# Performance work log

Measured on AMD Instinct MI355X. Metric: run time of the kernel, lower is better.

The kernel has to match this reference:

```python
import jax, jax.numpy as jnp
import numpy as np
import math

B, T, H, W, C = 2, 8, 32, 32, 512
DEPTH = 2
HEADS = 16
GH = 8            # global FAVOR+ heads (first GH heads, as in performer-pytorch)
DH = C // HEADS   # 32
WIN = C // 8      # 64 = local window size
FF = 2 * C
NB_F = int(DH * math.log(DH))  # 110 random features (performer default)


def _ortho_proj(m, d, rng):
    # gaussian orthogonal random matrix, scaling=0 (row norms ~ chi(d))
    blocks = []
    for _ in range(m // d + 1):
        q, _ = np.linalg.qr(rng.standard_normal((d, d)))
        blocks.append(q.T)
    Q = np.concatenate(blocks, 0)[:m]
    mult = np.linalg.norm(rng.standard_normal((m, d)), axis=1)
    return (mult[:, None] * Q).astype(np.float32)


def setup_inputs():
    rng = np.random.default_rng(0)
    g = lambda *s: jnp.asarray(rng.standard_normal(s) * 0.02, jnp.float32)
    z = lambda *s: jnp.zeros(s, jnp.float32)
    o = lambda *s: jnp.ones(s, jnp.float32)
    p = {}
    p["x"] = jnp.asarray(rng.standard_normal((B, T, H, W, C)), jnp.float32)
    p["ln1_g"], p["ln1_b"] = o(DEPTH, C), z(DEPTH, C)
    p["Wq"], p["bq"] = g(DEPTH, C, C), z(DEPTH, C)
    p["Wk"], p["bk"] = g(DEPTH, C, C), z(DEPTH, C)
    p["Wv"], p["bv"] = g(DEPTH, C, C), z(DEPTH, C)
    p["Wo"], p["bo"] = g(DEPTH, C, C), z(DEPTH, C)
    p["proj"] = jnp.asarray(np.stack([_ortho_proj(NB_F, DH, rng) for _ in range(DEPTH)]))
    p["ln2_g"], p["ln2_b"] = o(DEPTH, C), z(DEPTH, C)
    p["W1"], p["b1"] = g(DEPTH, C, FF), z(DEPTH, FF)
    p["W2"], p["b2"] = g(DEPTH, FF, C), z(DEPTH, C)
    return p


def _ln(x, g, b):
    m = x.mean(-1, keepdims=True)
    v = x.var(-1, keepdims=True)
    return (x - m) / jnp.sqrt(v + 1e-5) * g + b


def _softmax_kernel(x, proj, is_query):
    # FAVOR+ positive softmax features. x: [b,h,n,d], proj: [m,d]
    d = x.shape[-1]
    m = proj.shape[0]
    dn = d ** -0.25
    dd = jnp.einsum('bhnd,md->bhnm', x * dn, proj)
    diag = jnp.sum(x * x, -1, keepdims=True) * 0.5 * (dn * dn)
    if is_query:
        stab = jnp.max(dd, axis=-1, keepdims=True)
    else:
        stab = jnp.max(dd, axis=(-1, -2), keepdims=True)
    return (m ** -0.5) * (jnp.exp(dd - diag - stab) + 1e-4)


def _rot_half(x):
    x1, x2 = jnp.split(x, 2, axis=-1)
    return jnp.concatenate([-x2, x1], axis=-1)


def _local_attn(q, k, v, win=WIN):
    # non-causal sliding window, look_backward=1, look_forward=1
    b, hh, n, d = q.shape
    nw = n // win
    qb = q.reshape(b, hh, nw, win, d)
    kb = k.reshape(b, hh, nw, win, d)
    vb = v.reshape(b, hh, nw, win, d)

    def look(t):
        p = jnp.pad(t, ((0, 0), (0, 0), (1, 1), (0, 0), (0, 0)))
        return jnp.concatenate([p[:, :, :-2], p[:, :, 1:-1], p[:, :, 2:]], 3)

    kk, vv = look(kb), look(vb)
    posb = jnp.arange(n).reshape(nw, win)
    pp = jnp.pad(posb, ((1, 1), (0, 0)), constant_values=-1)
    kpos = jnp.concatenate([pp[:-2], pp[1:-1], pp[2:]], 1)
    mask = (kpos == -1)[None, None, :, None, :]
    s = jnp.einsum('bhwid,bhwjd->bhwij', qb * (d ** -0.5), kk)
    s = jnp.where(mask, -1e9, s)
    a = jax.nn.softmax(s, axis=-1)
    o = jnp.einsum('bhwij,bhwjd->bhwid', a, vv)
    return o.reshape(b, hh, n, d)


def _forward(x, ln1_g, ln1_b, Wq, bq, Wk, bk, Wv, bv, Wo, bo, proj, ln2_g, ln2_b, W1, b1, W2, b2):
    Bx, Tx, Hx, Wx, Cx = x.shape
    n = Tx * Hx * Wx
    h = x.reshape(Bx, n, Cx)
    # rotary rel-pos for local heads (local-attention rel_pos_emb_config)
    inv_freq = 1.0 / (10000.0 ** (jnp.arange(0, DH, 2, dtype=jnp.float32) / DH))
    freqs = jnp.arange(n, dtype=jnp.float32)[:, None] * inv_freq[None, :]
    emb = jnp.concatenate([freqs, freqs], -1)
    sin, cos = jnp.sin(emb), jnp.cos(emb)

    for l in range(DEPTH):
        y = _ln(h, ln1_g[l], ln1_b[l])
        q = (y @ Wq[l] + bq[l]).reshape(Bx, n, HEADS, DH).transpose(0, 2, 1, 3)
        k = (y @ Wk[l] + bk[l]).reshape(Bx, n, HEADS, DH).transpose(0, 2, 1, 3)
        v = (y @ Wv[l] + bv[l]).reshape(Bx, n, HEADS, DH).transpose(0, 2, 1, 3)
        gq, lq = q[:, :GH], q[:, GH:]
        gk, lk = k[:, :GH], k[:, GH:]
        gv, lv = v[:, :GH], v[:, GH:]
        # global: FAVOR+ linear attention
        qp = _softmax_kernel(gq, proj[l], True)
        kp = _softmax_kernel(gk, proj[l], False)
        Dinv = 1.0 / jnp.einsum('bhnm,bhm->bhn', qp, kp.sum(-2))
        ctx = jnp.einsum('bhnm,bhnd->bhmd', kp, gv)
        og = jnp.einsum('bhmd,bhnm,bhn->bhnd', ctx, qp, Dinv)
        # local: windowed attention with rotary pos emb
        lqr = lq * cos + _rot_half(lq) * sin
        lkr = lk * cos + _rot_half(lk) * sin
        ol = _local_attn(lqr, lkr, lv)
        o = jnp.concatenate([og, ol], 1).transpose(0, 2, 1, 3).reshape(Bx, n, Cx)
        h = h + o @ Wo[l] + bo[l]
        y = _ln(h, ln2_g[l], ln2_b[l])
        h = h + jax.nn.gelu(y @ W1[l] + b1[l], approximate=False) @ W2[l] + b2[l]
    return h.reshape(Bx, Tx, Hx, Wx, Cx)


def reference(x, ln1_g, ln1_b, Wq, bq, Wk, bk, Wv, bv, Wo, bo, proj, ln2_g, ln2_b, W1, b1, W2, b2):
    return _forward(x, ln1_g, ln1_b, Wq, bq, Wk, bk, Wv, bv, Wo, bo, proj, ln2_g, ln2_b, W1, b1, W2, b2)
```

## Files before the change

### kernel.cpp

```cpp
#include <hip/hip_runtime.h>
#include <math.h>

namespace {

constexpr int BATCH = 2;
constexpr int NTOK  = 8192;
constexpr int MROWS = 16384;
constexpr int C     = 512;
constexpr int GH    = 8;
constexpr int DH    = 32;
constexpr int WIN   = 64;
constexpr int NW    = 128;
constexpr int FF    = 1024;
constexpr int NBF   = 110;
constexpr int NBFP  = 128;

constexpr float F_DN     = 0.42044820762685725f;
constexpr float F_RNORM  = 0.09534625892455924f;
constexpr float F_LSCALE = 0.17677669529663687f;

typedef __attribute__((ext_vector_type(8))) short bf16x8;
typedef __attribute__((ext_vector_type(4))) float f32x4;

__device__ __forceinline__ ushort f2b(float f){
  unsigned u = __float_as_uint(f);
  unsigned r = u + 0x7FFFu + ((u >> 16) & 1u);
  return (ushort)(r >> 16);
}
__device__ __forceinline__ float b2f(ushort u){
  return __uint_as_float((unsigned)u << 16);
}

__device__ __forceinline__ void gload16(const void* g, void* l){
  __builtin_amdgcn_global_load_lds((const __attribute__((address_space(1))) void*)g,
                                   (__attribute__((address_space(3))) void*)l, 16, 0, 0);
}

__global__ void k_tables(float* __restrict__ cost, float* __restrict__ sint){
  int idx = blockIdx.x*256 + threadIdx.x;
  if (idx >= NTOK*16) return;
  int pos = idx >> 4, f = idx & 15;
  float inv = powf(10000.f, -(float)f/16.f);
  float ang = (float)pos * inv;
  cost[idx] = cosf(ang);
  sint[idx] = sinf(ang);
}

__global__ __launch_bounds__(256) void k_wcvt_all(const float* __restrict__ Wq, const float* __restrict__ Wk,
     const float* __restrict__ Wv, const float* __restrict__ Wo, const float* __restrict__ W1,
     const float* __restrict__ W2, ushort* __restrict__ wt){
  __shared__ float t[32][33];
  int id = blockIdx.x;
  int l = id >> 11;
  int r = id & 2047;
  const float* src; ushort* dst; int K, N, bx, by;
  if (r < 1024){
    int mat = r >> 8, tt = r & 255;
    bx = tt & 15; by = tt >> 4; K = 512; N = 512;
    src = ((mat == 0) ? Wq : (mat == 1) ? Wk : (mat == 2) ? Wv : Wo) + (size_t)l*262144;
    dst = wt + (size_t)l*2097152 + (size_t)mat*262144;
  } else if (r < 1536){
    int tt = r - 1024;
    bx = tt & 31; by = tt >> 5; K = 512; N = 1024;
    src = W1 + (size_t)l*524288;
    dst = wt + (size_t)l*2097152 + 1048576;
  } else {
    int tt = r - 1536;
    bx = tt & 15; by = tt >> 4; K = 1024; N = 512;
    src = W2 + (size_t)l*524288;
    dst = wt + (size_t)l*2097152 + 1572864;
  }
  int tx = threadIdx.x & 31, ty = threadIdx.x >> 5;
  #pragma unroll
  for (int rr = ty; rr < 32; rr += 8) t[rr][tx] = src[(size_t)(by*32+rr)*N + bx*32 + tx];
  __syncthreads();
  #pragma unroll
  for (int rr = ty; rr < 32; rr += 8) dst[(size_t)(bx*32+rr)*K + by*32 + tx] = f2b(t[tx][rr]);
}

__global__ __launch_bounds__(256) void k_ln(const float* __restrict__ x, const float* __restrict__ g,
                     const float* __restrict__ b, ushort* __restrict__ y){
  int row = blockIdx.x, t = threadIdx.x;
  const float* xr = x + (size_t)row*C;
  float2 v = *(const float2*)(xr + 2*t);
  float s = v.x + v.y, ss = v.x*v.x + v.y*v.y;
  #pragma unroll
  for (int o = 32; o; o >>= 1){ s += __shfl_down(s, o); ss += __shfl_down(ss, o); }
  __shared__ float rs[4], rss[4];
  int wv = t >> 6, ln = t & 63;
  if (ln == 0){ rs[wv] = s; rss[wv] = ss; }
  __syncthreads();
  float S = rs[0]+rs[1]+rs[2]+rs[3], SS = rss[0]+rss[1]+rss[2]+rss[3];
  float mean = S * (1.f/C);
  float var  = SS * (1.f/C) - mean*mean;
  float rstd = rsqrtf(var + 1e-5f);
  float2 gg = *(const float2*)(g + 2*t);
  float2 bb = *(const float2*)(b + 2*t);
  ushort2 ov;
  ov.x = f2b((v.x - mean)*rstd*gg.x + bb.x);
  ov.y = f2b((v.y - mean)*rstd*gg.y + bb.y);
  *(ushort2*)(y + (size_t)row*C + 2*t) = ov;
}

template<int ACT, int OBF, int QKV>
__global__ __launch_bounds__(256) void k_mgemm(const ushort* __restrict__ A, const ushort* __restrict__ Bt,
      const float* __restrict__ bias, const float* __restrict__ bias2, const float* __restrict__ bias3,
      const float* __restrict__ res, float* __restrict__ outf, ushort* __restrict__ outb,
      const float* __restrict__ cosT, const float* __restrict__ sinT, int Nd, int Kd){
  __shared__ ushort As[128*32];
  __shared__ ushort Bs[128*32];
  int tid = threadIdx.x;
  int lane = tid & 63, wave = tid >> 6;
  int wr = wave >> 1, wc = wave & 1;
  int gx = gridDim.x;
  int nwg = gx * (int)gridDim.y;
  int bid = (int)(blockIdx.y*gx + blockIdx.x);
  int swz = (bid & 7)*(nwg >> 3) + (bid >> 3);
  int row0 = (swz / gx)*128, col0 = (swz % gx)*128;
  f32x4 acc[4][4] = {};
  for (int k0 = 0; k0 < Kd; k0 += 32){
    __syncthreads();
    #pragma unroll
    for (int c = 0; c < 2; c++){
      int off = (wave*2 + c)*1024 + lane*16;
      int r = off >> 6, ke = (off & 63) >> 1;
      gload16(A  + (size_t)(row0 + r)*Kd + k0 + ke, (char*)As + (wave*2 + c)*1024);
      gload16(Bt + (size_t)(col0 + r)*Kd + k0 + ke, (char*)Bs + (wave*2 + c)*1024);
    }
    __syncthreads();
    bf16x8 af[4], bfr[4];
    #pragma unroll
    for (int m = 0; m < 4; m++)
      af[m] = *(const bf16x8*)((const char*)As + (wr*64 + m*16 + (lane&15))*64 + (lane>>4)*16);
    #pragma unroll
    for (int n = 0; n < 4; n++)
      bfr[n] = *(const bf16x8*)((const char*)Bs + (wc*64 + n*16 + (lane&15))*64 + (lane>>4)*16);
    #pragma unroll
    for (int m = 0; m < 4; m++)
      #pragma unroll
      for (int n = 0; n < 4; n++)
        acc[m][n] = __builtin_amdgcn_mfma_f32_16x16x32_bf16(af[m], bfr[n], acc[m][n], 0, 0, 0);
  }
  if (QKV){
    #pragma unroll
    for (int m = 0; m < 4; m++){
      int rbase = row0 + wr*64 + m*16 + (lane>>4)*4;
      #pragma unroll
      for (int np = 0; np < 2; np++){
        int n0 = 2*np, n1 = n0 + 1;
        int ccol = col0 + wc*64 + n0*16 + (lane&15);
        int bid2 = ccol >> 9;
        int cl  = ccol & 511;
        const float* bp = (bid2 == 0) ? bias : (bid2 == 1) ? bias2 : bias3;
        float b0 = bp[cl], b1 = bp[cl+16];
        bool dorope = (bid2 < 2) && (cl >= 256);
        ushort* obase = outb + (size_t)bid2*MROWS*C;
        int d = lane & 15;
        #pragma unroll
        for (int r = 0; r < 4; r++){
          int grow = rbase + r;
          float a  = acc[m][n0][r] + b0;
          float bb = acc[m][n1][r] + b1;
          if (dorope){
            int pos = grow & (NTOK-1);
            float cv = cosT[pos*16 + d], sv = sinT[pos*16 + d];
            float na = a*cv - bb*sv;
            float nb = bb*cv + a*sv;
            a = na; bb = nb;
          }
          obase[(size_t)grow*C + cl]      = f2b(a);
          obase[(size_t)grow*C + cl + 16] = f2b(bb);
        }
      }
    }
    return;
  }
  #pragma unroll
  for (int m = 0; m < 4; m++){
    int rbase = row0 + wr*64 + m*16 + (lane>>4)*4;
    #pragma unroll
    for (int n = 0; n < 4; n++){
      int ccol = col0 + wc*64 + n*16 + (lane&15);
      float bv = bias[ccol];
      #pragma unroll
      for (int r = 0; r < 4; r++){
        int grow = rbase + r;
        float vv = acc[m][n][r] + bv;
        if (ACT == 1) vv = 0.5f*vv*(1.f + erff(vv*0.7071067811865476f));
        if (res) vv += res[(size_t)grow*Nd + ccol];
        if (OBF) outb[(size_t)grow*Nd + ccol] = f2b(vv);
        else     outf[(size_t)grow*Nd + ccol] = vv;
      }
    }
  }
}

__global__ __launch_bounds__(256) void k_kpre2(const ushort* __restrict__ k, const float* __restrict__ proj,
        float* __restrict__ diag, float* __restrict__ bmax){
  int bh = blockIdx.x >> 5, chunk = blockIdx.x & 31;
  int b = bh >> 3, h = bh & 7;
  __shared__ __align__(16) ushort pl[NBFP*40];
  __shared__ float red[4];
  int tid = threadIdx.x, lane = tid & 63, wave = tid >> 6;
  int c = lane & 15, g = lane >> 4;
  for (int idx = tid; idx < NBFP*32; idx += 256){
    int f = idx >> 5, d = idx & 31;
    pl[f*40 + d] = (f < NBF) ? f2b(proj[idx]*F_DN) : (ushort)0;
  }
  __syncthreads();
  const ushort* kbase = k + ((size_t)b*NTOK + chunk*256)*C + h*DH;
  f32x4 zz = {0.f, 0.f, 0.f, 0.f};
  float mx = -1e30f;
  #pragma unroll
  for (int s = 0; s < 4; s++){
    bf16x8 af = *(const bf16x8*)(kbase + (size_t)(s*64 + wave*16 + c)*C + g*8);
    const ushort* ap = (const ushort*)&af;
    float sq = 0.f;
    #pragma unroll
    for (int j = 0; j < 8; j++){ float vv = b2f(ap[j]); sq += vv*vv; }
    sq += __shfl_xor(sq, 16);
    sq += __shfl_xor(sq, 32);
    if (g == 0) diag[bh*NTOK + chunk*256 + s*64 + wave*16 + c] = 0.5f*F_DN*F_DN*sq;
    #pragma unroll
    for (int ft = 0; ft < 8; ft++){
      bf16x8 bf = *(const bf16x8*)(pl + (ft*16 + c)*40 + g*8);
      f32x4 dd = __builtin_amdgcn_mfma_f32_16x16x32_bf16(af, bf, zz, 0, 0, 0);
      if (ft*16 + c < NBF)
        mx = fmaxf(mx, fmaxf(fmaxf(dd[0], dd[1]), fmaxf(dd[2], dd[3])));
    }
  }
  #pragma unroll
  for (int o = 1; o < 64; o <<= 1) mx = fmaxf(mx, __shfl_xor(mx, o));
  if (lane == 0) red[wave] = mx;
  __syncthreads();
  if (tid == 0) bmax[bh*32 + chunk] = fmaxf(fmaxf(red[0],red[1]), fmaxf(red[2],red[3]));
}

__global__ void k_redmax(const float* __restrict__ bmax, float* __restrict__ stabf){
  int bh = blockIdx.x, t = threadIdx.x;
  float v = (t < 32) ? bmax[bh*32 + t] : -1e30f;
  #pragma unroll
  for (int o = 32; o; o >>= 1) v = fmaxf(v, __shfl_down(v, o));
  if (t == 0) stabf[bh] = v;
}

__global__ __launch_bounds__(256) void k_ctx3(const ushort* __restrict__ k, const ushort* __restrict__ v,
        const float* __restrict__ proj, const float* __restrict__ diag, const float* __restrict__ stabf,
        float* __restrict__ ctxp, float* __restrict__ ksump){
  int bh = blockIdx.x >> 5, chunk = blockIdx.x & 31;
  int b = bh >> 3, h = bh & 7;
  __shared__ __align__(16) ushort pl[NBFP*40];
  __shared__ __align__(16) ushort Ps[NBFP*72];
  __shared__ __align__(16) ushort Vt[48*72];
  __shared__ float dgl[256];
  int tid = threadIdx.x;
  int lane = tid & 63, wave = tid >> 6;
  int c = lane & 15, g = lane >> 4;
  int i0 = chunk*256;

  for (int idx = tid; idx < NBFP*32; idx += 256){
    int f = idx >> 5, d = idx & 31;
    pl[f*40 + d] = (f < NBF) ? f2b(proj[f*32 + d]*F_DN) : (ushort)0;
  }
  dgl[tid] = diag[bh*NTOK + i0 + tid];
  for (int idx = tid; idx < 15*72; idx += 256) Vt[33*72 + idx] = 0;
  float stab_v = stabf[bh];

  const ushort* kbase = k + ((size_t)b*NTOK + i0)*C + h*DH;
  const ushort* vbase = v + ((size_t)b*NTOK + i0)*C + h*DH;
  f32x4 zz = {0.f, 0.f, 0.f, 0.f};
  f32x4 acc[2][3] = {};

  for (int s = 0; s < 4; s++){
    __syncthreads();
    {
      int r = tid >> 2, part = tid & 3;
      uint4 vv = *(const uint4*)(vbase + (size_t)(s*64 + r)*C + part*8);
      const ushort* vp = (const ushort*)&vv;
      #pragma unroll
      for (int j = 0; j < 8; j++) Vt[(part*8+j)*72 + r] = vp[j];
      if (tid < 64) Vt[32*72 + tid] = 0x3F80;
    }
    bf16x8 af = *(const bf16x8*)(kbase + (size_t)(s*64 + wave*16 + c)*C + g*8);
    #pragma unroll
    for (int ft = 0; ft < 8; ft++){
      bf16x8 bf = *(const bf16x8*)(pl + (ft*16 + c)*40 + g*8);
      f32x4 dd = __builtin_amdgcn_mfma_f32_16x16x32_bf16(af, bf, zz, 0, 0, 0);
      int feat = ft*16 + c;
      bool fvalid = feat < NBF;
      ushort pb[4];
      #pragma unroll
      for (int r = 0; r < 4; r++){
        float kp = 0.f;
        if (fvalid){
          float dg_ = dgl[s*64 + wave*16 + g*4 + r];
          kp = F_RNORM*(__expf(dd[r] - dg_ - stab_v) + 1e-4f);
        }
        pb[r] = f2b(kp);
      }
      uint2 pd;
      pd.x = (unsigned)pb[0] | ((unsigned)pb[1] << 16);
      pd.y = (unsigned)pb[2] | ((unsigned)pb[3] << 16);
      *(uint2*)(Ps + (ft*16 + c)*72 + wave*16 + g*4) = pd;
    }
    __syncthreads();
    #pragma unroll
    for (int i = 0; i < 2; i++){
      int ft = wave*2 + i;
      #pragma unroll
      for (int kk = 0; kk < 2; kk++){
        bf16x8 ap = *(const bf16x8*)(Ps + (ft*16 + c)*72 + kk*32 + g*8);
        #pragma unroll
        for (int nt = 0; nt < 3; nt++){
          bf16x8 bv = *(const bf16x8*)(Vt + (nt*16 + c)*72 + kk*32 + g*8);
          acc[i][nt] = __builtin_amdgcn_mfma_f32_16x16x32_bf16(ap, bv, acc[i][nt], 0, 0, 0);
        }
      }
    }
  }
  size_t pbase = (size_t)(bh*32 + chunk)*NBF;
  #pragma unroll
  for (int i = 0; i < 2; i++){
    int ftb = (wave*2 + i)*16;
    #pragma unroll
    for (int r = 0; r < 4; r++){
      int feat = ftb + g*4 + r;
      if (feat < NBF){
        #pragma unroll
        for (int nt = 0; nt < 2; nt++)
          ctxp[(pbase + feat)*DH + nt*16 + c] = acc[i][nt][r];
        if (c == 0) ksump[pbase + feat] = acc[i][2][r];
      }
    }
  }
}

__global__ void k_ctxred(const float* __restrict__ ctxp, const float* __restrict__ ksump,
                         float* __restrict__ ctx, float* __restrict__ ksum){
  int bh = blockIdx.x / NBF, m = blockIdx.x % NBF;
  int t = threadIdx.x;
  if (t < DH){
    float s = 0.f;
    for (int c = 0; c < 32; c++) s += ctxp[((size_t)(bh*32 + c)*NBF + m)*DH + t];
    ctx[((size_t)bh*NBF + m)*DH + t] = s;
  } else if (t == DH){
    float s = 0.f;
    for (int c = 0; c < 32; c++) s += ksump[(size_t)(bh*32 + c)*NBF + m];
    ksum[bh*NBF + m] = s;
  }
}

__global__ __launch_bounds__(256) void k_qattn3(const ushort* __restrict__ q, const float* __restrict__ proj,
        const float* __restrict__ ctx, const float* __restrict__ ksum, ushort* __restrict__ o){
  int bh = blockIdx.x >> 7, chunk = blockIdx.x & 127;
  int b = bh >> 3, h = bh & 7;
  __shared__ __align__(16) ushort pl[NBFP*40];
  __shared__ __align__(16) ushort ql[64*40];
  __shared__ __align__(16) ushort ctl[32*136];
  __shared__ __align__(16) ushort Ps[64*136];
  __shared__ float ksl[NBFP];
  __shared__ float dgl[64];
  __shared__ float dvl[64];
  int tid = threadIdx.x;
  int lane = tid & 63, wave = tid >> 6;
  int c = lane & 15, g = lane >> 4;
  int i0 = chunk*64;

  for (int idx = tid; idx < NBFP*32; idx += 256){
    int f = idx >> 5, d = idx & 31;
    pl[f*40 + d] = (f < NBF) ? f2b(proj[f*32 + d]*F_DN) : (ushort)0;
  }
  {
    int row = tid >> 2, part = tid & 3;
    uint4 qq = *(const uint4*)(q + (size_t)(b*NTOK + i0 + row)*C + h*DH + part*8);
    *(uint4*)(ql + row*40 + part*8) = qq;
    const ushort* qp_ = (const ushort*)&qq;
    float sq = 0.f;
    #pragma unroll
    for (int j = 0; j < 8; j++){ float vv = b2f(qp_[j]); sq += vv*vv; }
    sq += __shfl_xor(sq, 1);
    sq += __shfl_xor(sq, 2);
    if (part == 0) dgl[row] = 0.5f*F_DN*F_DN*sq;
  }
  for (int idx = tid; idx < 32*NBFP; idx += 256){
    int d = idx >> 7, f = idx & 127;
    float vv = (f < NBF) ? ctx[((size_t)bh*NBF + f)*DH + d] : 0.f;
    ctl[d*136 + f] = f2b(vv);
  }
  if (tid < NBFP) ksl[tid] = (tid < NBF) ? ksum[bh*NBF + tid] : 0.f;
  __syncthreads();

  f32x4 zz = {0.f, 0.f, 0.f, 0.f};
  bf16x8 qf = *(const bf16x8*)(ql + (wave*16 + c)*40 + g*8);
  f32x4 st[8];
  #pragma unroll
  for (int mt = 0; mt < 8; mt++){
    bf16x8 af = *(const bf16x8*)(pl + (mt*16 + c)*40 + g*8);
    st[mt] = __builtin_amdgcn_mfma_f32_16x16x32_bf16(af, qf, zz, 0, 0, 0);
  }
  float mx = -1e30f;
  #pragma unroll
  for (int mt = 0; mt < 8; mt++)
    #pragma unroll
    for (int r = 0; r < 4; r++){
      int feat = mt*16 + g*4 + r;
      if (feat < NBF) mx = fmaxf(mx, st[mt][r]);
    }
  mx = fmaxf(mx, __shfl_xor(mx, 16));
  mx = fmaxf(mx, __shfl_xor(mx, 32));
  float diagv = dgl[wave*16 + c];
  float dv = 0.f;
  #pragma unroll
  for (int mt = 0; mt < 8; mt++){
    ushort pb[4];
    #pragma unroll
    for (int r = 0; r < 4; r++){
      int feat = mt*16 + g*4 + r;
      float qp = 0.f;
      if (feat < NBF) qp = F_RNORM*(__expf(st[mt][r] - diagv - mx) + 1e-4f);
      ushort qb = f2b(qp);
      pb[r] = qb;
      dv += b2f(qb)*ksl[feat];
    }
    uint2 pd;
    pd.x = (unsigned)pb[0] | ((unsigned)pb[1] << 16);
    pd.y = (unsigned)pb[2] | ((unsigned)pb[3] << 16);
    *(uint2*)(Ps + (wave*16 + c)*136 + mt*16 + g*4) = pd;
  }
  dv += __shfl_xor(dv, 16);
  dv += __shfl_xor(dv, 32);
  if (g == 0) dvl[wave*16 + c] = 1.f/dv;
  __syncthreads();

  #pragma unroll
  for (int n = 0; n < 2; n++){
    f32x4 acc = zz;
    #pragma unroll
    for (int kk = 0; kk < 4; kk++){
      bf16x8 ap = *(const bf16x8*)(Ps  + (wave*16 + c)*136 + kk*32 + g*8);
      bf16x8 bc = *(const bf16x8*)(ctl + (n*16 + c)*136    + kk*32 + g*8);
      acc = __builtin_amdgcn_mfma_f32_16x16x32_bf16(ap, bc, acc, 0, 0, 0);
    }
    #pragma unroll
    for (int r = 0; r < 4; r++){
      int qrow = wave*16 + g*4 + r;
      float val = acc[r]*dvl[qrow];
      o[(size_t)(b*NTOK + i0 + qrow)*C + h*DH + n*16 + c] = f2b(val);
    }
  }
}

__global__ __launch_bounds__(256) void k_local2(const ushort* __restrict__ q, const ushort* __restrict__ k,
        const ushort* __restrict__ v, ushort* __restrict__ o){
  int blk = blockIdx.x;
  int w = blk & (NW-1);
  int rem = blk >> 7;
  int hl = rem & 7, b = rem >> 3;
  int hd = GH + hl;
  __shared__ __align__(16) ushort Ks[192*32];
  __shared__ __align__(16) ushort Vt[32*200];
  __shared__ __align__(16) ushort Ps[4*16*200];
  int tid = threadIdx.x;
  int lane = tid & 63, wave = tid >> 6;
  int c = lane & 15, g = lane >> 4;

  const ushort* kbase = k + (size_t)b*NTOK*C + hd*DH;
  const ushort* vbase = v + (size_t)b*NTOK*C + hd*DH;
  #pragma unroll
  for (int s = 0; s < 3; s++){
    int ch = tid + s*256;
    int row = ch >> 2, part = ch & 3;
    int kp = min(max((w-1)*WIN + row, 0), NTOK-1);
    gload16(kbase + (size_t)kp*C + part*8, (char*)Ks + (s*256 + wave*64)*16);
  }
  #pragma unroll
  for (int s = 0; s < 3; s++){
    int ch = tid + s*256;
    int row = ch >> 2, part = ch & 3;
    int kp = min(max((w-1)*WIN + row, 0), NTOK-1);
    uint4 vv = *(const uint4*)(vbase + (size_t)kp*C + part*8);
    const ushort* vp = (const ushort*)&vv;
    #pragma unroll
    for (int j = 0; j < 8; j++) Vt[(part*8+j)*200 + row] = vp[j];
  }
  int qrow = w*WIN + wave*16 + c;
  bf16x8 qf = *(const bf16x8*)(q + ((size_t)b*NTOK + qrow)*C + hd*DH + g*8);
  asm volatile("s_waitcnt vmcnt(0)" ::: "memory");
  __syncthreads();

  f32x4 zz = {0.f, 0.f, 0.f, 0.f};
  f32x4 st[12];
  #pragma unroll
  for (int t = 0; t < 12; t++){
    bf16x8 af = *(const bf16x8*)(Ks + (16*t + c)*32 + g*8);
    st[t] = __builtin_amdgcn_mfma_f32_16x16x32_bf16(af, qf, zz, 0, 0, 0);
  }
  int t0 = (w == 0) ? 4 : 0;
  int t1 = (w == NW-1) ? 8 : 12;
  float lsum = 0.f;
  ushort* pw = Ps + wave*3200 + c*200;
  #pragma unroll
  for (int t = 0; t < 12; t++){
    bool valid = (t >= t0) && (t < t1);
    float p0 = valid ? __expf(st[t][0]*F_LSCALE) : 0.f;
    float p1 = valid ? __expf(st[t][1]*F_LSCALE) : 0.f;
    float p2 = valid ? __expf(st[t][2]*F_LSCALE) : 0.f;
    float p3 = valid ? __expf(st[t][3]*F_LSCALE) : 0.f;
    lsum += (p0+p1)+(p2+p3);
    uint2 pd;
    pd.x = (unsigned)f2b(p0) | ((unsigned)f2b(p1) << 16);
    pd.y = (unsigned)f2b(p2) | ((unsigned)f2b(p3) << 16);
    *(uint2*)(pw + 16*t + 4*g) = pd;
  }
  lsum += __shfl_xor(lsum, 16);
  lsum += __shfl_xor(lsum, 32);

  f32x4 oc0 = zz, oc1 = zz;
  #pragma unroll
  for (int kb = 0; kb < 6; kb++){
    bf16x8 pf = *(const bf16x8*)(pw + kb*32 + g*8);
    bf16x8 v0 = *(const bf16x8*)(Vt + c*200 + kb*32 + g*8);
    bf16x8 v1 = *(const bf16x8*)(Vt + (16 + c)*200 + kb*32 + g*8);
    oc0 = __builtin_amdgcn_mfma_f32_16x16x32_bf16(v0, pf, oc0, 0, 0, 0);
    oc1 = __builtin_amdgcn_mfma_f32_16x16x32_bf16(v1, pf, oc1, 0, 0, 0);
  }
  float inv = 1.f/lsum;
  ushort* orow = o + ((size_t)b*NTOK + qrow)*C + hd*DH;
  uint2 w0, w1;
  w0.x = (unsigned)f2b(oc0[0]*inv) | ((unsigned)f2b(oc0[1]*inv) << 16);
  w0.y = (unsigned)f2b(oc0[2]*inv) | ((unsigned)f2b(oc0[3]*inv) << 16);
  w1.x = (unsigned)f2b(oc1[0]*inv) | ((unsigned)f2b(oc1[1]*inv) << 16);
  w1.y = (unsigned)f2b(oc1[2]*inv) | ((unsigned)f2b(oc1[3]*inv) << 16);
  *(uint2*)(orow + 4*g)      = w0;
  *(uint2*)(orow + 16 + 4*g) = w1;
}

}

extern "C" void kernel_launch(void* const* d_in, const int* in_sizes, int n_in,
                              void* d_out, int out_size, void* d_ws, size_t ws_size,
                              hipStream_t stream){
  (void)in_sizes; (void)n_in; (void)out_size; (void)ws_size;
  const float* x     = (const float*)d_in[0];
  const float* ln1_g = (const float*)d_in[1];
  const float* ln1_b = (const float*)d_in[2];
  const float* Wq    = (const float*)d_in[3];
  const float* bq    = (const float*)d_in[4];
  const float* Wk    = (const float*)d_in[5];
  const float* bk    = (const float*)d_in[6];
  const float* Wv    = (const float*)d_in[7];
  const float* bv    = (const float*)d_in[8];
  const float* Wo    = (const float*)d_in[9];
  const float* bo    = (const float*)d_in[10];
  const float* proj  = (const float*)d_in[11];
  const float* ln2_g = (const float*)d_in[12];
  const float* ln2_b = (const float*)d_in[13];
  const float* W1    = (const float*)d_in[14];
  const float* b1    = (const float*)d_in[15];
  const float* W2    = (const float*)d_in[16];
  const float* b2    = (const float*)d_in[17];

  float* h = (float*)d_out;
  const size_t MC = (size_t)MROWS*C;
  char* w = (char*)d_ws;
  auto alloc = [&](size_t bytes)->char*{ char* p = w; w += (bytes + 255) & ~(size_t)255; return p; };

  ushort* y16  = (ushort*)alloc(MC*2);
  ushort* qb16 = (ushort*)alloc(MC*2);
  ushort* kb16 = (ushort*)alloc(MC*2);
  ushort* vb16 = (ushort*)alloc(MC*2);
  ushort* o16  = (ushort*)alloc(MC*2);
  ushort* wt   = (ushort*)alloc((size_t)2*2097152*2);
  float*  cost = (float*) alloc((size_t)NTOK*16*4);
  float*  sint = (float*) alloc((size_t)NTOK*16*4);
  float*  diag = (float*) alloc((size_t)16*NTOK*4);
  float*  bmax = (float*) alloc(16*32*4);
  float*  stabf= (float*) alloc(16*4);
  float*  ctxb = (float*) alloc((size_t)16*NBF*DH*4);
  float*  ksum = (float*) alloc((size_t)16*NBF*4);

  ushort* mid16 = qb16;
  float*  ctxp  = (float*)o16;
  float*  ksump = ctxp + (size_t)16*32*NBF*DH;

  k_tables<<<(NTOK*16 + 255)/256, 256, 0, stream>>>(cost, sint);
  k_wcvt_all<<<4096, 256, 0, stream>>>(Wq, Wk, Wv, Wo, W1, W2, wt);

  dim3 blk(256);
  dim3 g512(4, 128);
  dim3 gqkv(12, 128);
  dim3 gff(8, 128);

  for (int l = 0; l < 2; l++){
    const float* pj = proj + (size_t)l*NBF*DH;
    ushort* wl  = wt + (size_t)l*2097152;
    ushort* wtq = wl;
    ushort* wto = wl +  786432;
    ushort* wt1 = wl + 1048576;
    ushort* wt2 = wl + 1572864;
    const float* hin = (l == 0) ? x : h;

    k_ln<<<MROWS, 256, 0, stream>>>(hin, ln1_g + l*C, ln1_b + l*C, y16);
    k_mgemm<0,1,1><<<gqkv, blk, 0, stream>>>(y16, wtq, bq + l*C, bk + l*C, bv + l*C,
                                             nullptr, nullptr, qb16, cost, sint, 1536, C);
    k_kpre2<<<16*32, 256, 0, stream>>>(kb16, pj, diag, bmax);
    k_redmax<<<16, 64, 0, stream>>>(bmax, stabf);
    k_ctx3<<<16*32, 256, 0, stream>>>(kb16, vb16, pj, diag, stabf, ctxp, ksump);
    k_ctxred<<<16*NBF, 64, 0, stream>>>(ctxp, ksump, ctxb, ksum);
    k_qattn3<<<16*128, 256, 0, stream>>>(qb16, pj, ctxb, ksum, o16);
    k_local2<<<BATCH*8*NW, 256, 0, stream>>>(qb16, kb16, vb16, o16);
    k_mgemm<0,0,0><<<g512, blk, 0, stream>>>(o16, wto, bo + l*C, nullptr, nullptr, hin, h, nullptr,
                                             nullptr, nullptr, C, C);
    k_ln<<<MROWS, 256, 0, stream>>>(h, ln2_g + l*C, ln2_b + l*C, y16);
    k_mgemm<1,1,0><<<gff, blk, 0, stream>>>(y16, wt1, b1 + l*FF, nullptr, nullptr, nullptr,
                                            nullptr, mid16, nullptr, nullptr, FF, C);
    k_mgemm<0,0,0><<<g512, blk, 0, stream>>>(mid16, wt2, b2 + l*C, nullptr, nullptr, h, h, nullptr,
                                             nullptr, nullptr, C, FF);
  }
}
```

Measured before the change: 562.9 us.

## Double-buffer LDS tiles in MFMA GEMM to overlap loads with compute

The GEMM main loop now keeps two LDS buffers for the A and B tiles. It issues the global-to-LDS loads for the next K tile right after reading fragments of the current one, then runs the MFMAs, with one barrier per iteration instead of two. It also raises wave priority around the MFMA block via s_setprio. The aim is to hide global load latency behind matrix math, at the cost of doubling LDS use per block, which may reduce occupancy.

```diff
diff --git a/kernel.cpp b/kernel.cpp
--- a/kernel.cpp
+++ b/kernel.cpp
@@ -107,8 +107,8 @@
       const float* __restrict__ bias, const float* __restrict__ bias2, const float* __restrict__ bias3,
       const float* __restrict__ res, float* __restrict__ outf, ushort* __restrict__ outb,
       const float* __restrict__ cosT, const float* __restrict__ sinT, int Nd, int Kd){
-  __shared__ ushort As[128*32];
-  __shared__ ushort Bs[128*32];
+  __shared__ ushort As[2][128*32];
+  __shared__ ushort Bs[2][128*32];
   int tid = threadIdx.x;
   int lane = tid & 63, wave = tid >> 6;
   int wr = wave >> 1, wc = wave & 1;
@@ -118,29 +118,45 @@
   int swz = (bid & 7)*(nwg >> 3) + (bid >> 3);
   int row0 = (swz / gx)*128, col0 = (swz % gx)*128;
   f32x4 acc[4][4] = {};
-  for (int k0 = 0; k0 < Kd; k0 += 32){
-    __syncthreads();
-    #pragma unroll
-    for (int c = 0; c < 2; c++){
-      int off = (wave*2 + c)*1024 + lane*16;
-      int r = off >> 6, ke = (off & 63) >> 1;
-      gload16(A  + (size_t)(row0 + r)*Kd + k0 + ke, (char*)As + (wave*2 + c)*1024);
-      gload16(Bt + (size_t)(col0 + r)*Kd + k0 + ke, (char*)Bs + (wave*2 + c)*1024);
-    }
-    __syncthreads();
+  int nt = Kd >> 5;
+
+  #define STAGE(buf, kt) {                                                        \
+    int k0_ = (kt)*32;                                                            \
+    _Pragma("unroll")                                                             \
+    for (int cc = 0; cc < 2; cc++){                                               \
+      int off = (wave*2 + cc)*1024 + lane*16;                                     \
+      int r_ = off >> 6, ke_ = (off & 63) >> 1;                                   \
+      gload16(A  + (size_t)(row0 + r_)*Kd + k0_ + ke_,                            \
+              (char*)As[buf] + (wave*2 + cc)*1024);                               \
+      gload16(Bt + (size_t)(col0 + r_)*Kd + k0_ + ke_,                            \
+              (char*)Bs[buf] + (wave*2 + cc)*1024);                               \
+    }                                                                             \
+  }
+
+  STAGE(0, 0);
+  __syncthreads();
+
+  for (int t = 0; t < nt; t++){
+    int cur = t & 1;
     bf16x8 af[4], bfr[4];
     #pragma unroll
     for (int m = 0; m < 4; m++)
-      af[m] = *(const bf16x8*)((const char*)As + (wr*64 + m*16 + (lane&15))*64 + (lane>>4)*16);
+      af[m] = *(const bf16x8*)((const char*)As[cur] + (wr*64 + m*16 + (lane&15))*64 + (lane>>4)*16);
     #pragma unroll
     for (int n = 0; n < 4; n++)
-      bfr[n] = *(const bf16x8*)((const char*)Bs + (wc*64 + n*16 + (lane&15))*64 + (lane>>4)*16);
+      bfr[n] = *(const bf16x8*)((const char*)Bs[cur] + (wc*64 + n*16 + (lane&15))*64 + (lane>>4)*16);
+    if (t + 1 < nt) STAGE(cur^1, t+1);
+    __builtin_amdgcn_s_setprio(1);
     #pragma unroll
     for (int m = 0; m < 4; m++)
       #pragma unroll
       for (int n = 0; n < 4; n++)
         acc[m][n] = __builtin_amdgcn_mfma_f32_16x16x32_bf16(af[m], bfr[n], acc[m][n], 0, 0, 0);
-  }
+    __builtin_amdgcn_s_setprio(0);
+    __syncthreads();
+  }
+  #undef STAGE
+
   if (QKV){
     #pragma unroll
     for (int m = 0; m < 4; m++){
```

Result: faster. 522.5 us (-7.2%).
